# Performance work log

Measured on AMD Instinct MI355X. Metric: run time of the kernel, lower is better.

## Reference

```python
import jax, jax.numpy as jnp
import numpy as np

B, T, K, H = 4, 2048, 128, 8
MASK = True


def setup_inputs() -> dict:
    key = jax.random.key(0)
    ks = jax.random.split(key, 6)
    s = 0.02
    return {
        "x": jax.random.normal(ks[0], (B, T, K), dtype=jnp.float32),
        "Wq": jax.random.normal(ks[1], (K, H * K), dtype=jnp.float32) * s,
        "Wk": jax.random.normal(ks[2], (K, H * K), dtype=jnp.float32) * s,
        "Wv": jax.random.normal(ks[3], (K, H * K), dtype=jnp.float32) * s,
        "Wu": jax.random.normal(ks[4], (H * K, K), dtype=jnp.float32) * s,
        "bu": jnp.zeros((K,), dtype=jnp.float32),
    }


def reference(x, Wq, Wk, Wv, Wu, bu):
    b, t, k = x.shape
    h = H
    q = (x @ Wq).reshape(b, t, h, k)
    kk = (x @ Wk).reshape(b, t, h, k)
    # module pre-scales values by k**-0.25 (idiosyncratic but faithful)
    v = (x @ Wv).reshape(b, t, h, k) * (k ** -0.25)
    # scores [b, h, t, t], scaled by k**-0.5
    scores = jnp.einsum('bthd,bshd->bhts', q, kk) * (k ** -0.5)
    if MASK:
        causal = jnp.tril(jnp.ones((t, t), dtype=bool))
        scores = jnp.where(causal, scores, -jnp.inf)
    w = jax.nn.softmax(scores, axis=-1)
    out = jnp.einsum('bhts,bshd->bthd', w, v).reshape(b, t, h * k)
    return out @ Wu + bu
```

## Files before the change

kernel.cpp:

```cpp
#include <hip/hip_runtime.h>
#include <hip/hip_bf16.h>
#include <math.h>

#define B_ 4
#define T_ 2048
#define D_ 128
#define H_ 8
#define BT_ (B_*T_)
#define HD_ (H_*D_)

typedef __attribute__((ext_vector_type(8))) short bf16x8;
typedef __attribute__((ext_vector_type(4))) float f32x4;

__device__ __forceinline__ short f2bf(float f) {
  union { float f; unsigned u; } v; v.f = f;
  return (short)((v.u + 0x8000u) >> 16);
}

#if __has_builtin(__builtin_amdgcn_exp2f)
#define EXP2F(x) __builtin_amdgcn_exp2f(x)
#else
#define EXP2F(x) exp2f(x)
#endif

#define QSCALE 0.12752040242046492f
#define VSCALE 0.29730177875068026f

__device__ __forceinline__ void gld16(const short* g, short* l) {
  __builtin_amdgcn_global_load_lds(
      (const __attribute__((address_space(1))) void*)g,
      (__attribute__((address_space(3))) void*)l, 16, 0, 0);
}

__global__ __launch_bounds__(256) void prep(
    const float* __restrict__ x, const float* __restrict__ Wq,
    const float* __restrict__ Wk, const float* __restrict__ Wv,
    short* __restrict__ xbf, short* __restrict__ WT)
{
  __shared__ __align__(16) short Tt[128*128];
  const int tid = threadIdx.x;
  const int id = blockIdx.x;
  if (id < 24) {
    const int wsel = id >> 3, nt = id & 7;
    const float* W = (wsel == 0) ? Wq : (wsel == 1) ? Wk : Wv;
    #pragma unroll 4
    for (int i = tid; i < 4096; i += 256) {
      int k = i >> 5, n4 = (i & 31) << 2;
      float4 v = *(const float4*)&W[(size_t)k * HD_ + nt*128 + n4];
      float vv[4] = {v.x, v.y, v.z, v.w};
      #pragma unroll
      for (int j = 0; j < 4; j++) {
        int n = n4 + j;
        Tt[n*128 + (((k >> 3) ^ (n & 15)) << 3) + (k & 7)] = f2bf(vv[j]);
      }
    }
    __syncthreads();
    #pragma unroll 2
    for (int i = tid; i < 2048; i += 256) {
      int n = i >> 4, c = i & 15;
      *(bf16x8*)&WT[((size_t)wsel*1024 + nt*128 + n)*128 + (c << 3)] =
          *(bf16x8*)&Tt[n*128 + ((c ^ (n & 15)) << 3)];
    }
  } else {
    const int xb = id - 24;
    const float4* xs = (const float4*)x + (size_t)xb * 2048;
    short4* xd = (short4*)xbf + (size_t)xb * 2048;
    #pragma unroll 8
    for (int i = tid; i < 2048; i += 256) {
      float4 v = xs[i];
      short4 p; p.x = f2bf(v.x); p.y = f2bf(v.y); p.z = f2bf(v.z); p.w = f2bf(v.w);
      xd[i] = p;
    }
  }
}

__global__ __launch_bounds__(256) void qkv_proj(
    const short* __restrict__ xbf, const short* __restrict__ WT,
    short* __restrict__ Qw, short* __restrict__ Kw, short* __restrict__ Vw)
{
  __shared__ __align__(16) short As[128*128];
  __shared__ __align__(16) short Bs[128*128];
  const int tid = threadIdx.x;
  const int m0 = blockIdx.x * 128;
  const int ng0 = blockIdx.y * 128;

  #pragma unroll 4
  for (int i = tid; i < 2048; i += 256) {
    int row = i >> 4, c = i & 15;
    *(bf16x8*)&As[row*128 + ((c ^ (row & 15)) << 3)] =
        *(const bf16x8*)(xbf + (size_t)(m0 + row)*128 + (c << 3));
  }
  #pragma unroll 4
  for (int i = tid; i < 2048; i += 256) {
    int n = i >> 4, c = i & 15;
    *(bf16x8*)&Bs[n*128 + ((c ^ (n & 15)) << 3)] =
        *(const bf16x8*)(WT + (size_t)(ng0 + n)*128 + (c << 3));
  }
  __syncthreads();

  const int w = tid >> 6, lane = tid & 63, quad = lane >> 4, l16 = lane & 15;
  const int wm = (w & 1) * 64, wn = (w >> 1) * 64;

  f32x4 acc[4][4];
  #pragma unroll
  for (int a = 0; a < 4; a++)
    #pragma unroll
    for (int b = 0; b < 4; b++) acc[a][b] = (f32x4){0.f, 0.f, 0.f, 0.f};

  #pragma unroll
  for (int kk = 0; kk < 4; kk++) {
    const int swz = ((kk*4 + quad) ^ l16) << 3;
    bf16x8 af[4], bfv[4];
    #pragma unroll
    for (int mi = 0; mi < 4; mi++) af[mi]  = *(bf16x8*)&As[(wm + mi*16 + l16)*128 + swz];
    #pragma unroll
    for (int ni = 0; ni < 4; ni++) bfv[ni] = *(bf16x8*)&Bs[(wn + ni*16 + l16)*128 + swz];
    #pragma unroll
    for (int mi = 0; mi < 4; mi++)
      #pragma unroll
      for (int ni = 0; ni < 4; ni++)
        acc[mi][ni] = __builtin_amdgcn_mfma_f32_16x16x32_bf16(af[mi], bfv[ni], acc[mi][ni], 0, 0, 0);
  }

  const int wsel = (int)blockIdx.y >> 3;
  const int n0 = ((int)blockIdx.y & 7) * 128;
  #pragma unroll
  for (int mi = 0; mi < 4; mi++) {
    #pragma unroll
    for (int ni = 0; ni < 4; ni++) {
      const int mrow0 = m0 + wm + mi*16 + quad*4;
      const int ncol  = n0 + wn + ni*16 + l16;
      const int h = ncol >> 7, d = ncol & 127;
      const int b = mrow0 >> 11;
      const int bhh = b*H_ + h;
      if (wsel == 2) {
        const int t0 = mrow0 & 2047;
        const int tile = t0 >> 6, tl0 = t0 & 63;
        const size_t base = ((size_t)bhh*32 + tile) * 8192;
        short4 p;
        p.x = f2bf(acc[mi][ni][0] * VSCALE);
        p.y = f2bf(acc[mi][ni][1] * VSCALE);
        p.z = f2bf(acc[mi][ni][2] * VSCALE);
        p.w = f2bf(acc[mi][ni][3] * VSCALE);
        *(short4*)&Vw[base + (((d << 3) | ((tl0 >> 3) ^ (d & 7))) << 3) + (tl0 & 7)] = p;
      } else if (wsel == 1) {
        #pragma unroll
        for (int r = 0; r < 4; r++) {
          const int t = (mrow0 + r) & 2047;
          const int tile = t >> 6, tl = t & 63;
          const size_t base = ((size_t)bhh*32 + tile) * 8192;
          Kw[base + ((((tl << 4) | ((d >> 3) ^ (tl & 15)))) << 3) + (d & 7)] =
              f2bf(acc[mi][ni][r]);
        }
      } else {
        #pragma unroll
        for (int r = 0; r < 4; r++) {
          const int t = (mrow0 + r) & 2047;
          Qw[((size_t)bhh*T_ + t)*D_ + d] = f2bf(acc[mi][ni][r] * QSCALE);
        }
      }
    }
  }
}

__global__ __launch_bounds__(256, 4) void attn_kernel(
    const short* __restrict__ Qw, const short* __restrict__ Kw,
    const short* __restrict__ Vw, short* __restrict__ attnw)
{
  __shared__ __align__(16) short Ks[64*128];
  __shared__ __align__(16) short Vs[128*64];
  __shared__ __align__(16) short Ps[4*16*64];

  const int tid = threadIdx.x;
  const int id = (int)blockIdx.x;
  const int xcd = id & 7;
  const int j   = id >> 3;
  const int u   = j & 3;
  const int q   = (j >> 2) & 7;
  const int vv  = (j >> 5) & 3;
  const int slot = u ^ vv;
  const int qi = (slot == 0) ? q : (slot == 1) ? 15 - q
               : (slot == 2) ? 16 + q : 31 - q;
  const int bh = xcd | (u << 3);
  const int b = bh >> 3, h = bh & 7;
  const int w = tid >> 6, lane = tid & 63, quad = lane >> 4, l16 = lane & 15;
  const int rowQ = qi*64 + w*16;

  const short* Qp = Qw + (size_t)bh * T_ * D_;
  const short* Kp = Kw + (size_t)bh * T_ * D_;
  const short* Vp = Vw + (size_t)bh * D_ * T_;

  bf16x8 qa[4];
  #pragma unroll
  for (int kk = 0; kk < 4; kk++)
    qa[kk] = *(const bf16x8*)(Qp + (size_t)(rowQ + l16)*D_ + kk*32 + quad*8);

  f32x4 o[8];
  #pragma unroll
  for (int e = 0; e < 8; e++) o[e] = (f32x4){0,0,0,0};
  float l[4] = {0,0,0,0};

  short* Pw = &Ps[w*16*64];
  const int nIter = qi + 1;

  for (int it = 0; it < nIter; ++it) {
    if (it) __syncthreads();
    {
      const short* kt = Kp + ((size_t)it << 13);
      const short* vt = Vp + ((size_t)it << 13);
      const int wo = w*2048 + lane*8;
      #pragma unroll
      for (int cc = 0; cc < 4; cc++) {
        gld16(kt + wo + cc*512, &Ks[w*2048 + cc*512]);
        gld16(vt + wo + cc*512, &Vs[w*2048 + cc*512]);
      }
    }
    __syncthreads();

    f32x4 s[4];
    #pragma unroll
    for (int nj = 0; nj < 4; nj++) s[nj] = (f32x4){0,0,0,0};
    #pragma unroll
    for (int kk = 0; kk < 4; kk++) {
      const int swz = ((kk*4 + quad) ^ l16) << 3;
      #pragma unroll
      for (int nj = 0; nj < 4; nj++) {
        bf16x8 kb = *(bf16x8*)&Ks[(nj*16 + l16)*128 + swz];
        s[nj] = __builtin_amdgcn_mfma_f32_16x16x32_bf16(qa[kk], kb, s[nj], 0, 0, 0);
      }
    }

    if (it < qi) {
      #pragma unroll
      for (int nj = 0; nj < 4; nj++) {
        #pragma unroll
        for (int r = 0; r < 4; r++) {
          float p = EXP2F(s[nj][r]);
          l[r] += p;
          const int row = quad*4 + r, col = nj*16 + l16;
          Pw[row*64 + (((col >> 3) ^ (row & 7)) << 3) + (col & 7)] = f2bf(p);
        }
      }
    } else {
      const int s0 = it * 64;
      #pragma unroll
      for (int nj = 0; nj < 4; nj++) {
        const int key = s0 + nj*16 + l16;
        #pragma unroll
        for (int r = 0; r < 4; r++) {
          float p = (key > rowQ + quad*4 + r) ? 0.f : EXP2F(s[nj][r]);
          l[r] += p;
          const int row = quad*4 + r, col = nj*16 + l16;
          Pw[row*64 + (((col >> 3) ^ (row & 7)) << 3) + (col & 7)] = f2bf(p);
        }
      }
    }

    #pragma unroll
    for (int kk2 = 0; kk2 < 2; kk2++) {
      const int swz = ((kk2*4 + quad) ^ (l16 & 7)) << 3;
      bf16x8 pa = *(bf16x8*)&Pw[l16*64 + swz];
      #pragma unroll
      for (int e = 0; e < 8; e++) {
        bf16x8 vb = *(const bf16x8*)&Vs[(e*16 + l16)*64 + swz];
        o[e] = __builtin_amdgcn_mfma_f32_16x16x32_bf16(pa, vb, o[e], 0, 0, 0);
      }
    }
    __syncthreads();
  }

  #pragma unroll
  for (int r = 0; r < 4; r++) {
    float t = l[r];
    t += __shfl_xor(t, 1); t += __shfl_xor(t, 2);
    t += __shfl_xor(t, 4); t += __shfl_xor(t, 8);
    l[r] = 1.0f / t;
  }
  #pragma unroll
  for (int e = 0; e < 8; e++) {
    #pragma unroll
    for (int r = 0; r < 4; r++) {
      const int t = rowQ + quad*4 + r;
      attnw[((size_t)(b*T_ + t))*HD_ + h*D_ + e*16 + l16] = f2bf(o[e][r] * l[r]);
    }
  }
}

__global__ __launch_bounds__(256) void wu_transpose(
    const float* __restrict__ Wu, short* __restrict__ WuT)
{
  __shared__ __align__(16) short Tt[128*128];
  const int tid = threadIdx.x;
  const int k0 = blockIdx.x * 128;
  #pragma unroll 4
  for (int i = tid; i < 4096; i += 256) {
    int k = i >> 5, n4 = (i & 31) << 2;
    float4 v = *(const float4*)&Wu[(size_t)(k0 + k) * D_ + n4];
    float vv[4] = {v.x, v.y, v.z, v.w};
    #pragma unroll
    for (int jj = 0; jj < 4; jj++) {
      int n = n4 + jj;
      Tt[n*128 + (((k >> 3) ^ (n & 15)) << 3) + (k & 7)] = f2bf(vv[jj]);
    }
  }
  __syncthreads();
  #pragma unroll 2
  for (int i = tid; i < 2048; i += 256) {
    int n = i >> 4, cc = i & 15;
    *(bf16x8*)&WuT[(size_t)n * HD_ + k0 + (cc << 3)] =
        *(bf16x8*)&Tt[n*128 + ((cc ^ (n & 15)) << 3)];
  }
}

__global__ __launch_bounds__(256) void out_proj(
    const short* __restrict__ attnw, const short* __restrict__ WuT,
    float* __restrict__ pws)
{
  __shared__ __align__(16) short As2[32*128];
  __shared__ __align__(16) short Bs2[128*128];
  const int tid = threadIdx.x;
  const int m0 = blockIdx.x * 32;
  const int kh = blockIdx.y;
  const int w = tid >> 6, lane = tid & 63, quad = lane >> 4, l16 = lane & 15;
  const int rw = (w & 1) * 16, eh = (w >> 1) * 4;

  f32x4 o[4];
  #pragma unroll
  for (int e = 0; e < 4; e++) o[e] = (f32x4){0.f, 0.f, 0.f, 0.f};

  for (int kc = 0; kc < 4; kc++) {
    const int kbase = kh*512 + kc*128;
    if (kc) __syncthreads();
    #pragma unroll 2
    for (int i = tid; i < 512; i += 256) {
      int row = i >> 4, cc = i & 15;
      *(bf16x8*)&As2[row*128 + ((cc ^ (row & 15)) << 3)] =
          *(const bf16x8*)(attnw + (size_t)(m0 + row)*HD_ + kbase + (cc << 3));
    }
    #pragma unroll 8
    for (int i = tid; i < 2048; i += 256) {
      int n = i >> 4, cc = i & 15;
      *(bf16x8*)&Bs2[n*128 + ((cc ^ (n & 15)) << 3)] =
          *(const bf16x8*)(WuT + (size_t)n*HD_ + kbase + (cc << 3));
    }
    __syncthreads();
    #pragma unroll
    for (int kk = 0; kk < 4; kk++) {
      const int swz = ((kk*4 + quad) ^ l16) << 3;
      bf16x8 a = *(bf16x8*)&As2[(rw + l16)*128 + swz];
      #pragma unroll
      for (int e = 0; e < 4; e++) {
        bf16x8 bfr = *(bf16x8*)&Bs2[((eh + e)*16 + l16)*128 + swz];
        o[e] = __builtin_amdgcn_mfma_f32_16x16x32_bf16(a, bfr, o[e], 0, 0, 0);
      }
    }
  }

  float* dst = pws + (size_t)kh * BT_ * D_;
  #pragma unroll
  for (int e = 0; e < 4; e++) {
    const int n = (eh + e)*16 + l16;
    #pragma unroll
    for (int r = 0; r < 4; r++) {
      const int m = m0 + rw + quad*4 + r;
      dst[(size_t)m*D_ + n] = o[e][r];
    }
  }
}

__global__ __launch_bounds__(256) void reduce_bias(
    const float* __restrict__ pws, const float* __restrict__ bu,
    float* __restrict__ out)
{
  const int base = ((int)blockIdx.x * 256 + (int)threadIdx.x) * 4;
  const float4* p0 = (const float4*)pws;
  const float4* p1 = (const float4*)(pws + (size_t)BT_ * D_);
  const float4* b4 = (const float4*)bu;
  float4* o4 = (float4*)out;
  #pragma unroll
  for (int jj = 0; jj < 4; jj++) {
    int i = base + jj;
    float4 a = p0[i], b = p1[i], c = b4[i & 31];
    float4 r; r.x = a.x + b.x + c.x; r.y = a.y + b.y + c.y;
    r.z = a.z + b.z + c.z; r.w = a.w + b.w + c.w;
    o4[i] = r;
  }
}

extern "C" void kernel_launch(void* const* d_in, const int* in_sizes, int n_in,
                              void* d_out, int out_size, void* d_ws, size_t ws_size,
                              hipStream_t stream) {
  (void)in_sizes; (void)n_in; (void)out_size; (void)ws_size;
  const float* x  = (const float*)d_in[0];
  const float* Wq = (const float*)d_in[1];
  const float* Wk = (const float*)d_in[2];
  const float* Wv = (const float*)d_in[3];
  const float* Wu = (const float*)d_in[4];
  const float* bu = (const float*)d_in[5];
  float* out = (float*)d_out;

  const size_t headElems = (size_t)B_ * H_ * T_ * D_;
  short* Qw    = (short*)d_ws;
  short* Kw    = Qw + headElems;
  short* Vw    = Kw + headElems;
  short* attnw = Vw + headElems;
  short* xbf = attnw;
  short* WT  = attnw + (size_t)BT_ * D_;
  short* WuT = Kw;
  float* pws = (float*)Qw;

  prep<<<dim3(152), 256, 0, stream>>>(x, Wq, Wk, Wv, xbf, WT);
  qkv_proj<<<dim3(64, 24), 256, 0, stream>>>(xbf, WT, Qw, Kw, Vw);
  attn_kernel<<<dim3(1024), 256, 0, stream>>>(Qw, Kw, Vw, attnw);
  wu_transpose<<<dim3(8), 256, 0, stream>>>(Wu, WuT);
  out_proj<<<dim3(256, 2), 256, 0, stream>>>(attnw, WuT, pws);
  reduce_bias<<<dim3(256), 256, 0, stream>>>(pws, bu, out);
}
```

Baseline: 166.9 us.

## Pre-tile operands, double-buffer attention and out-proj loads, fuse bias reduce

Intermediate tensors (x, weights, Q/K/V, attention output) are now written in pre-swizzled tile-contiguous layouts, so the consuming kernels can use direct global-to-LDS copies and coalesced stores through shared memory. The attention kernel pairs a low and a high query tile per block to balance the causal work, and double-buffers K/V tiles so the next tile loads while the current one is computed. The output projection now runs the full K reduction in one kernel with double-buffered loads and adds the bias directly, which removes the split-K partial buffer and the separate reduce kernel. The cost is more shared memory per block, lower occupancy bounds, and a serial two-phase loop per attention block.

Measured after the change: 160.3 us. 1.04x faster.

```diff
diff --git a/kernel.cpp b/kernel.cpp
--- a/kernel.cpp
+++ b/kernel.cpp
@@ -6,8 +6,8 @@
 #define T_ 2048
 #define D_ 128
 #define H_ 8
-#define BT_ (B_*T_)
-#define HD_ (H_*D_)
+#define BT_ 8192
+#define HD_ 1024
 
 typedef __attribute__((ext_vector_type(8))) short bf16x8;
 typedef __attribute__((ext_vector_type(4))) float f32x4;
@@ -55,52 +55,48 @@
       }
     }
     __syncthreads();
+    short* dst = WT + (size_t)id * 16384;
     #pragma unroll 2
-    for (int i = tid; i < 2048; i += 256) {
-      int n = i >> 4, c = i & 15;
-      *(bf16x8*)&WT[((size_t)wsel*1024 + nt*128 + n)*128 + (c << 3)] =
-          *(bf16x8*)&Tt[n*128 + ((c ^ (n & 15)) << 3)];
-    }
+    for (int i = tid; i < 2048; i += 256)
+      *(bf16x8*)&dst[i*8] = *(bf16x8*)&Tt[i*8];
   } else {
     const int xb = id - 24;
-    const float4* xs = (const float4*)x + (size_t)xb * 2048;
-    short4* xd = (short4*)xbf + (size_t)xb * 2048;
-    #pragma unroll 8
-    for (int i = tid; i < 2048; i += 256) {
-      float4 v = xs[i];
-      short4 p; p.x = f2bf(v.x); p.y = f2bf(v.y); p.z = f2bf(v.z); p.w = f2bf(v.w);
-      xd[i] = p;
-    }
-  }
-}
-
-__global__ __launch_bounds__(256) void qkv_proj(
+    const float* xs = x + (size_t)xb * 16384;
+    short* dst = xbf + (size_t)xb * 16384;
+    #pragma unroll 4
+    for (int i = tid; i < 4096; i += 256) {
+      float4 v = ((const float4*)xs)[i];
+      int row = i >> 5, c = (i & 31) >> 1, half = i & 1;
+      short4 p;
+      p.x = f2bf(v.x); p.y = f2bf(v.y); p.z = f2bf(v.z); p.w = f2bf(v.w);
+      *(short4*)&dst[(row*16 + (c ^ (row & 15)))*8 + half*4] = p;
+    }
+  }
+}
+
+__global__ __launch_bounds__(256, 2) void qkv_proj(
     const short* __restrict__ xbf, const short* __restrict__ WT,
     short* __restrict__ Qw, short* __restrict__ Kw, short* __restrict__ Vw)
 {
-  __shared__ __align__(16) short As[128*128];
-  __shared__ __align__(16) short Bs[128*128];
+  __shared__ __align__(16) short As[16384];
+  __shared__ __align__(16) short Bs[16384];
   const int tid = threadIdx.x;
+  const int w = tid >> 6, lane = tid & 63, quad = lane >> 4, l16 = lane & 15;
   const int m0 = blockIdx.x * 128;
-  const int ng0 = blockIdx.y * 128;
-
-  #pragma unroll 4
-  for (int i = tid; i < 2048; i += 256) {
-    int row = i >> 4, c = i & 15;
-    *(bf16x8*)&As[row*128 + ((c ^ (row & 15)) << 3)] =
-        *(const bf16x8*)(xbf + (size_t)(m0 + row)*128 + (c << 3));
-  }
-  #pragma unroll 4
-  for (int i = tid; i < 2048; i += 256) {
-    int n = i >> 4, c = i & 15;
-    *(bf16x8*)&Bs[n*128 + ((c ^ (n & 15)) << 3)] =
-        *(const bf16x8*)(WT + (size_t)(ng0 + n)*128 + (c << 3));
+
+  {
+    const short* asrc = xbf + (size_t)blockIdx.x * 16384;
+    const short* bsrc = WT + (size_t)blockIdx.y * 16384;
+    const int so = w*4096 + lane*8;
+    #pragma unroll
+    for (int cc = 0; cc < 8; cc++) {
+      gld16(asrc + so + cc*512, &As[w*4096 + cc*512]);
+      gld16(bsrc + so + cc*512, &Bs[w*4096 + cc*512]);
+    }
   }
   __syncthreads();
 
-  const int w = tid >> 6, lane = tid & 63, quad = lane >> 4, l16 = lane & 15;
   const int wm = (w & 1) * 64, wn = (w >> 1) * 64;
-
   f32x4 acc[4][4];
   #pragma unroll
   for (int a = 0; a < 4; a++)
@@ -122,268 +118,267 @@
         acc[mi][ni] = __builtin_amdgcn_mfma_f32_16x16x32_bf16(af[mi], bfv[ni], acc[mi][ni], 0, 0, 0);
   }
 
+  __syncthreads();
   const int wsel = (int)blockIdx.y >> 3;
-  const int n0 = ((int)blockIdx.y & 7) * 128;
   #pragma unroll
   for (int mi = 0; mi < 4; mi++) {
     #pragma unroll
     for (int ni = 0; ni < 4; ni++) {
-      const int mrow0 = m0 + wm + mi*16 + quad*4;
-      const int ncol  = n0 + wn + ni*16 + l16;
-      const int h = ncol >> 7, d = ncol & 127;
-      const int b = mrow0 >> 11;
-      const int bhh = b*H_ + h;
-      if (wsel == 2) {
-        const int t0 = mrow0 & 2047;
-        const int tile = t0 >> 6, tl0 = t0 & 63;
-        const size_t base = ((size_t)bhh*32 + tile) * 8192;
-        short4 p;
-        p.x = f2bf(acc[mi][ni][0] * VSCALE);
-        p.y = f2bf(acc[mi][ni][1] * VSCALE);
-        p.z = f2bf(acc[mi][ni][2] * VSCALE);
-        p.w = f2bf(acc[mi][ni][3] * VSCALE);
-        *(short4*)&Vw[base + (((d << 3) | ((tl0 >> 3) ^ (d & 7))) << 3) + (tl0 & 7)] = p;
+      const int t0l = wm + mi*16 + quad*4;
+      const int d   = wn + ni*16 + l16;
+      if (wsel == 0) {
+        #pragma unroll
+        for (int r = 0; r < 4; r++)
+          As[(t0l + r)*128 + d] = f2bf(acc[mi][ni][r] * QSCALE);
       } else if (wsel == 1) {
+        const int c = d >> 3;
         #pragma unroll
         for (int r = 0; r < 4; r++) {
-          const int t = (mrow0 + r) & 2047;
-          const int tile = t >> 6, tl = t & 63;
-          const size_t base = ((size_t)bhh*32 + tile) * 8192;
-          Kw[base + ((((tl << 4) | ((d >> 3) ^ (tl & 15)))) << 3) + (d & 7)] =
+          const int tl = (t0l + r) & 63, tile = (t0l + r) >> 6;
+          As[tile*8192 + tl*128 + ((c ^ (tl & 15)) << 3) + (d & 7)] =
               f2bf(acc[mi][ni][r]);
         }
       } else {
         #pragma unroll
         for (int r = 0; r < 4; r++) {
-          const int t = (mrow0 + r) & 2047;
-          Qw[((size_t)bhh*T_ + t)*D_ + d] = f2bf(acc[mi][ni][r] * QSCALE);
-        }
-      }
-    }
-  }
-}
-
-__global__ __launch_bounds__(256, 4) void attn_kernel(
+          const int tl = (t0l + r) & 63, tile = (t0l + r) >> 6;
+          As[tile*8192 + d*64 + (((tl >> 3) ^ (d & 7)) << 3) + (tl & 7)] =
+              f2bf(acc[mi][ni][r] * VSCALE);
+        }
+      }
+    }
+  }
+  __syncthreads();
+
+  const int h = (int)blockIdx.y & 7;
+  const int b = m0 >> 11, t0 = m0 & 2047;
+  short* base = ((wsel == 0) ? Qw : (wsel == 1) ? Kw : Vw)
+              + (size_t)(b*H_ + h)*262144 + (size_t)t0*128;
+  #pragma unroll 2
+  for (int i = tid; i < 2048; i += 256)
+    *(bf16x8*)&base[i*8] = *(bf16x8*)&As[i*8];
+}
+
+__global__ __launch_bounds__(256, 2) void attn_kernel(
     const short* __restrict__ Qw, const short* __restrict__ Kw,
     const short* __restrict__ Vw, short* __restrict__ attnw)
 {
-  __shared__ __align__(16) short Ks[64*128];
-  __shared__ __align__(16) short Vs[128*64];
-  __shared__ __align__(16) short Ps[4*16*64];
+  __shared__ __align__(16) short Ks[2][8192];
+  __shared__ __align__(16) short Vs[2][8192];
+  __shared__ __align__(16) short Ps[4096];
 
   const int tid = threadIdx.x;
   const int id = (int)blockIdx.x;
   const int xcd = id & 7;
-  const int j   = id >> 3;
-  const int u   = j & 3;
-  const int q   = (j >> 2) & 7;
-  const int vv  = (j >> 5) & 3;
-  const int slot = u ^ vv;
-  const int qi = (slot == 0) ? q : (slot == 1) ? 15 - q
-               : (slot == 2) ? 16 + q : 31 - q;
+  const int u   = (id >> 3) & 3;
+  const int pid = id >> 5;
   const int bh = xcd | (u << 3);
   const int b = bh >> 3, h = bh & 7;
   const int w = tid >> 6, lane = tid & 63, quad = lane >> 4, l16 = lane & 15;
-  const int rowQ = qi*64 + w*16;
 
   const short* Qp = Qw + (size_t)bh * T_ * D_;
   const short* Kp = Kw + (size_t)bh * T_ * D_;
   const short* Vp = Vw + (size_t)bh * D_ * T_;
-
-  bf16x8 qa[4];
-  #pragma unroll
-  for (int kk = 0; kk < 4; kk++)
-    qa[kk] = *(const bf16x8*)(Qp + (size_t)(rowQ + l16)*D_ + kk*32 + quad*8);
-
-  f32x4 o[8];
-  #pragma unroll
-  for (int e = 0; e < 8; e++) o[e] = (f32x4){0,0,0,0};
-  float l[4] = {0,0,0,0};
-
-  short* Pw = &Ps[w*16*64];
-  const int nIter = qi + 1;
-
-  for (int it = 0; it < nIter; ++it) {
-    if (it) __syncthreads();
+  short* Pw = &Ps[w*1024];
+  const int so = w*2048 + lane*8;
+
+  #pragma unroll 1
+  for (int ph = 0; ph < 2; ph++) {
+    const int qi = ph ? (31 - pid) : pid;
+    const int rowQ = qi*64 + w*16;
+
+    bf16x8 qa[4];
+    #pragma unroll
+    for (int kk = 0; kk < 4; kk++)
+      qa[kk] = *(const bf16x8*)(Qp + (size_t)(rowQ + l16)*D_ + kk*32 + quad*8);
+
+    f32x4 o[8];
+    #pragma unroll
+    for (int e = 0; e < 8; e++) o[e] = (f32x4){0,0,0,0};
+    float l[4] = {0,0,0,0};
+
+    __syncthreads();
     {
-      const short* kt = Kp + ((size_t)it << 13);
-      const short* vt = Vp + ((size_t)it << 13);
-      const int wo = w*2048 + lane*8;
+      const short* kt = Kp;
+      const short* vt = Vp;
       #pragma unroll
       for (int cc = 0; cc < 4; cc++) {
-        gld16(kt + wo + cc*512, &Ks[w*2048 + cc*512]);
-        gld16(vt + wo + cc*512, &Vs[w*2048 + cc*512]);
-      }
-    }
-    __syncthreads();
-
-    f32x4 s[4];
-    #pragma unroll
-    for (int nj = 0; nj < 4; nj++) s[nj] = (f32x4){0,0,0,0};
-    #pragma unroll
-    for (int kk = 0; kk < 4; kk++) {
-      const int swz = ((kk*4 + quad) ^ l16) << 3;
-      #pragma unroll
-      for (int nj = 0; nj < 4; nj++) {
-        bf16x8 kb = *(bf16x8*)&Ks[(nj*16 + l16)*128 + swz];
-        s[nj] = __builtin_amdgcn_mfma_f32_16x16x32_bf16(qa[kk], kb, s[nj], 0, 0, 0);
-      }
-    }
-
-    if (it < qi) {
-      #pragma unroll
-      for (int nj = 0; nj < 4; nj++) {
-        #pragma unroll
-        for (int r = 0; r < 4; r++) {
-          float p = EXP2F(s[nj][r]);
-          l[r] += p;
-          const int row = quad*4 + r, col = nj*16 + l16;
-          Pw[row*64 + (((col >> 3) ^ (row & 7)) << 3) + (col & 7)] = f2bf(p);
-        }
-      }
-    } else {
-      const int s0 = it * 64;
-      #pragma unroll
-      for (int nj = 0; nj < 4; nj++) {
-        const int key = s0 + nj*16 + l16;
-        #pragma unroll
-        for (int r = 0; r < 4; r++) {
-          float p = (key > rowQ + quad*4 + r) ? 0.f : EXP2F(s[nj][r]);
-          l[r] += p;
-          const int row = quad*4 + r, col = nj*16 + l16;
-          Pw[row*64 + (((col >> 3) ^ (row & 7)) << 3) + (col & 7)] = f2bf(p);
-        }
-      }
-    }
-
-    #pragma unroll
-    for (int kk2 = 0; kk2 < 2; kk2++) {
-      const int swz = ((kk2*4 + quad) ^ (l16 & 7)) << 3;
-      bf16x8 pa = *(bf16x8*)&Pw[l16*64 + swz];
-      #pragma unroll
-      for (int e = 0; e < 8; e++) {
-        bf16x8 vb = *(const bf16x8*)&Vs[(e*16 + l16)*64 + swz];
-        o[e] = __builtin_amdgcn_mfma_f32_16x16x32_bf16(pa, vb, o[e], 0, 0, 0);
-      }
-    }
-    __syncthreads();
-  }
-
-  #pragma unroll
-  for (int r = 0; r < 4; r++) {
-    float t = l[r];
-    t += __shfl_xor(t, 1); t += __shfl_xor(t, 2);
-    t += __shfl_xor(t, 4); t += __shfl_xor(t, 8);
-    l[r] = 1.0f / t;
-  }
-  #pragma unroll
-  for (int e = 0; e < 8; e++) {
+        gld16(kt + so + cc*512, &Ks[0][w*2048 + cc*512]);
+        gld16(vt + so + cc*512, &Vs[0][w*2048 + cc*512]);
+      }
+    }
+    int buf = 0;
+
+    for (int it = 0; it <= qi; ++it) {
+      __syncthreads();
+      if (it < qi) {
+        const short* kt = Kp + ((size_t)(it+1) << 13);
+        const short* vt = Vp + ((size_t)(it+1) << 13);
+        #pragma unroll
+        for (int cc = 0; cc < 4; cc++) {
+          gld16(kt + so + cc*512, &Ks[buf^1][w*2048 + cc*512]);
+          gld16(vt + so + cc*512, &Vs[buf^1][w*2048 + cc*512]);
+        }
+      }
+      const short* ks = &Ks[buf][0];
+      const short* vs = &Vs[buf][0];
+
+      f32x4 s[4];
+      #pragma unroll
+      for (int nj = 0; nj < 4; nj++) s[nj] = (f32x4){0,0,0,0};
+      #pragma unroll
+      for (int kk = 0; kk < 4; kk++) {
+        const int swz = ((kk*4 + quad) ^ l16) << 3;
+        #pragma unroll
+        for (int nj = 0; nj < 4; nj++) {
+          bf16x8 kb = *(const bf16x8*)&ks[(nj*16 + l16)*128 + swz];
+          s[nj] = __builtin_amdgcn_mfma_f32_16x16x32_bf16(qa[kk], kb, s[nj], 0, 0, 0);
+        }
+      }
+
+      if (it < qi) {
+        #pragma unroll
+        for (int nj = 0; nj < 4; nj++) {
+          #pragma unroll
+          for (int r = 0; r < 4; r++) {
+            float p = EXP2F(s[nj][r]);
+            l[r] += p;
+            const int row = quad*4 + r, col = nj*16 + l16;
+            Pw[row*64 + (((col >> 3) ^ (row & 7)) << 3) + (col & 7)] = f2bf(p);
+          }
+        }
+      } else {
+        const int s0 = it * 64;
+        #pragma unroll
+        for (int nj = 0; nj < 4; nj++) {
+          const int key = s0 + nj*16 + l16;
+          #pragma unroll
+          for (int r = 0; r < 4; r++) {
+            float p = (key > rowQ + quad*4 + r) ? 0.f : EXP2F(s[nj][r]);
+            l[r] += p;
+            const int row = quad*4 + r, col = nj*16 + l16;
+            Pw[row*64 + (((col >> 3) ^ (row & 7)) << 3) + (col & 7)] = f2bf(p);
+          }
+        }
+      }
+
+      #pragma unroll
+      for (int kk2 = 0; kk2 < 2; kk2++) {
+        const int swz = ((kk2*4 + quad) ^ (l16 & 7)) << 3;
+        bf16x8 pa = *(bf16x8*)&Pw[l16*64 + swz];
+        #pragma unroll
+        for (int e = 0; e < 8; e++) {
+          bf16x8 vb = *(const bf16x8*)&vs[(e*16 + l16)*64 + swz];
+          o[e] = __builtin_amdgcn_mfma_f32_16x16x32_bf16(pa, vb, o[e], 0, 0, 0);
+        }
+      }
+      buf ^= 1;
+    }
+
     #pragma unroll
     for (int r = 0; r < 4; r++) {
-      const int t = rowQ + quad*4 + r;
-      attnw[((size_t)(b*T_ + t))*HD_ + h*D_ + e*16 + l16] = f2bf(o[e][r] * l[r]);
-    }
-  }
-}
-
-__global__ __launch_bounds__(256) void wu_transpose(
+      float t = l[r];
+      t += __shfl_xor(t, 1); t += __shfl_xor(t, 2);
+      t += __shfl_xor(t, 4); t += __shfl_xor(t, 8);
+      l[r] = 1.0f / t;
+    }
+    const size_t tb = ((size_t)((b*2048 + rowQ) >> 5) * 8 + h) * 4096;
+    const int row0 = rowQ & 31;
+    #pragma unroll
+    for (int e = 0; e < 8; e++) {
+      const int c = e*2 + (l16 >> 3);
+      #pragma unroll
+      for (int r = 0; r < 4; r++) {
+        const int row = row0 + quad*4 + r;
+        attnw[tb + row*128 + ((c ^ (row & 15)) << 3) + (l16 & 7)] =
+            f2bf(o[e][r] * l[r]);
+      }
+    }
+  }
+}
+
+__global__ __launch_bounds__(256) void wu_prep(
     const float* __restrict__ Wu, short* __restrict__ WuT)
 {
   __shared__ __align__(16) short Tt[128*128];
   const int tid = threadIdx.x;
-  const int k0 = blockIdx.x * 128;
+  const int kc = blockIdx.x;
   #pragma unroll 4
   for (int i = tid; i < 4096; i += 256) {
-    int k = i >> 5, n4 = (i & 31) << 2;
-    float4 v = *(const float4*)&Wu[(size_t)(k0 + k) * D_ + n4];
+    int kl = i >> 5, n4 = (i & 31) << 2;
+    float4 v = *(const float4*)&Wu[(size_t)(kc*128 + kl) * D_ + n4];
     float vv[4] = {v.x, v.y, v.z, v.w};
     #pragma unroll
-    for (int jj = 0; jj < 4; jj++) {
-      int n = n4 + jj;
-      Tt[n*128 + (((k >> 3) ^ (n & 15)) << 3) + (k & 7)] = f2bf(vv[jj]);
+    for (int j = 0; j < 4; j++) {
+      int n = n4 + j;
+      Tt[n*128 + (((kl >> 3) ^ (n & 15)) << 3) + (kl & 7)] = f2bf(vv[j]);
     }
   }
   __syncthreads();
+  short* dst = WuT + (size_t)kc * 16384;
   #pragma unroll 2
-  for (int i = tid; i < 2048; i += 256) {
-    int n = i >> 4, cc = i & 15;
-    *(bf16x8*)&WuT[(size_t)n * HD_ + k0 + (cc << 3)] =
-        *(bf16x8*)&Tt[n*128 + ((cc ^ (n & 15)) << 3)];
-  }
-}
-
-__global__ __launch_bounds__(256) void out_proj(
+  for (int i = tid; i < 2048; i += 256)
+    *(bf16x8*)&dst[i*8] = *(bf16x8*)&Tt[i*8];
+}
+
+__global__ __launch_bounds__(256, 2) void out_proj(
     const short* __restrict__ attnw, const short* __restrict__ WuT,
-    float* __restrict__ pws)
+    const float* __restrict__ bu, float* __restrict__ out)
 {
-  __shared__ __align__(16) short As2[32*128];
-  __shared__ __align__(16) short Bs2[128*128];
+  __shared__ __align__(16) short As2[2][2048];
+  __shared__ __align__(16) short Bs2[2][16384];
   const int tid = threadIdx.x;
-  const int m0 = blockIdx.x * 32;
-  const int kh = blockIdx.y;
   const int w = tid >> 6, lane = tid & 63, quad = lane >> 4, l16 = lane & 15;
-  const int rw = (w & 1) * 16, eh = (w >> 1) * 4;
-
-  f32x4 o[4];
-  #pragma unroll
-  for (int e = 0; e < 4; e++) o[e] = (f32x4){0.f, 0.f, 0.f, 0.f};
-
-  for (int kc = 0; kc < 4; kc++) {
-    const int kbase = kh*512 + kc*128;
-    if (kc) __syncthreads();
-    #pragma unroll 2
-    for (int i = tid; i < 512; i += 256) {
-      int row = i >> 4, cc = i & 15;
-      *(bf16x8*)&As2[row*128 + ((cc ^ (row & 15)) << 3)] =
-          *(const bf16x8*)(attnw + (size_t)(m0 + row)*HD_ + kbase + (cc << 3));
-    }
-    #pragma unroll 8
-    for (int i = tid; i < 2048; i += 256) {
-      int n = i >> 4, cc = i & 15;
-      *(bf16x8*)&Bs2[n*128 + ((cc ^ (n & 15)) << 3)] =
-          *(const bf16x8*)(WuT + (size_t)n*HD_ + kbase + (cc << 3));
-    }
+  const int m0 = (int)blockIdx.x * 16;
+  const int mtile32 = m0 >> 5, half = (m0 >> 4) & 1;
+
+  f32x4 o2[2];
+  o2[0] = (f32x4){0,0,0,0}; o2[1] = (f32x4){0,0,0,0};
+
+  {
+    const short* ab = attnw + (size_t)(mtile32*8 + 0)*4096 + half*2048;
+    const short* bb = WuT;
+    gld16(ab + w*512 + lane*8, &As2[0][w*512]);
+    #pragma unroll
+    for (int cc = 0; cc < 8; cc++)
+      gld16(bb + w*4096 + cc*512 + lane*8, &Bs2[0][w*4096 + cc*512]);
+  }
+  int buf = 0;
+
+  for (int kc = 0; kc < 8; kc++) {
     __syncthreads();
+    if (kc < 7) {
+      const short* ab = attnw + (size_t)(mtile32*8 + kc + 1)*4096 + half*2048;
+      const short* bb = WuT + (size_t)(kc + 1)*16384;
+      gld16(ab + w*512 + lane*8, &As2[buf^1][w*512]);
+      #pragma unroll
+      for (int cc = 0; cc < 8; cc++)
+        gld16(bb + w*4096 + cc*512 + lane*8, &Bs2[buf^1][w*4096 + cc*512]);
+    }
+    const short* as = &As2[buf][0];
+    const short* bs = &Bs2[buf][0];
     #pragma unroll
     for (int kk = 0; kk < 4; kk++) {
       const int swz = ((kk*4 + quad) ^ l16) << 3;
-      bf16x8 a = *(bf16x8*)&As2[(rw + l16)*128 + swz];
-      #pragma unroll
-      for (int e = 0; e < 4; e++) {
-        bf16x8 bfr = *(bf16x8*)&Bs2[((eh + e)*16 + l16)*128 + swz];
-        o[e] = __builtin_amdgcn_mfma_f32_16x16x32_bf16(a, bfr, o[e], 0, 0, 0);
-      }
-    }
-  }
-
-  float* dst = pws + (size_t)kh * BT_ * D_;
+      bf16x8 a = *(const bf16x8*)&as[l16*128 + swz];
+      #pragma unroll
+      for (int e = 0; e < 2; e++) {
+        bf16x8 bfr = *(const bf16x8*)&bs[((w*2 + e)*16 + l16)*128 + swz];
+        o2[e] = __builtin_amdgcn_mfma_f32_16x16x32_bf16(a, bfr, o2[e], 0, 0, 0);
+      }
+    }
+    buf ^= 1;
+  }
+
   #pragma unroll
-  for (int e = 0; e < 4; e++) {
-    const int n = (eh + e)*16 + l16;
+  for (int e = 0; e < 2; e++) {
+    const int n = (w*2 + e)*16 + l16;
+    const float bias = bu[n];
     #pragma unroll
     for (int r = 0; r < 4; r++) {
-      const int m = m0 + rw + quad*4 + r;
-      dst[(size_t)m*D_ + n] = o[e][r];
-    }
-  }
-}
-
-__global__ __launch_bounds__(256) void reduce_bias(
-    const float* __restrict__ pws, const float* __restrict__ bu,
-    float* __restrict__ out)
-{
-  const int base = ((int)blockIdx.x * 256 + (int)threadIdx.x) * 4;
-  const float4* p0 = (const float4*)pws;
-  const float4* p1 = (const float4*)(pws + (size_t)BT_ * D_);
-  const float4* b4 = (const float4*)bu;
-  float4* o4 = (float4*)out;
-  #pragma unroll
-  for (int jj = 0; jj < 4; jj++) {
-    int i = base + jj;
-    float4 a = p0[i], b = p1[i], c = b4[i & 31];
-    float4 r; r.x = a.x + b.x + c.x; r.y = a.y + b.y + c.y;
-    r.z = a.z + b.z + c.z; r.w = a.w + b.w + c.w;
-    o4[i] = r;
+      const int m = m0 + quad*4 + r;
+      out[(size_t)m*D_ + n] = o2[e][r] + bias;
+    }
   }
 }
 
@@ -405,14 +400,12 @@
   short* Vw    = Kw + headElems;
   short* attnw = Vw + headElems;
   short* xbf = attnw;
-  short* WT  = attnw + (size_t)BT_ * D_;
+  short* WT  = attnw + 1048576;
   short* WuT = Kw;
-  float* pws = (float*)Qw;
-
-  prep<<<dim3(152), 256, 0, stream>>>(x, Wq, Wk, Wv, xbf, WT);
+
+  prep<<<dim3(88), 256, 0, stream>>>(x, Wq, Wk, Wv, xbf, WT);
   qkv_proj<<<dim3(64, 24), 256, 0, stream>>>(xbf, WT, Qw, Kw, Vw);
-  attn_kernel<<<dim3(1024), 256, 0, stream>>>(Qw, Kw, Vw, attnw);
-  wu_transpose<<<dim3(8), 256, 0, stream>>>(Wu, WuT);
-  out_proj<<<dim3(256, 2), 256, 0, stream>>>(attnw, WuT, pws);
-  reduce_bias<<<dim3(256), 256, 0, stream>>>(pws, bu, out);
-}
+  attn_kernel<<<dim3(512), 256, 0, stream>>>(Qw, Kw, Vw, attnw);
+  wu_prep<<<dim3(8), 256, 0, stream>>>(Wu, WuT);
+  out_proj<<<dim3(512), 256, 0, stream>>>(attnw, WuT, bu, out);
+}
```
